# Kernel optimization log

Hardware: AMD Instinct MI355X
Metric: run time of the kernel (lower is better)

Reference implementation:

```python
import jax, jax.numpy as jnp
import numpy as np

B, V, N, S, F, H, K, STEPS = 8, 3, 400, 1200, 16, 32, 10, 12
ALPHA_FUSE = 0.8
NEG = -9e15


def setup_inputs() -> dict:
    key = jax.random.key(0)
    ks = jax.random.split(key, 16)
    g = lambda i, shape, s=0.1: jax.random.normal(ks[i], shape, jnp.float32) * s
    return {
        "feat": jax.random.normal(ks[0], (B, S, F), jnp.float32),
        "adj": jax.random.bernoulli(ks[1], 0.05, (B, V, S, S)).astype(jnp.float32),
        "dis_lab": jax.random.uniform(ks[2], (B, K), dtype=jnp.float32),
        "W_gat": g(3, (V, F, H), 0.3),
        "a_gat": g(4, (V, 2 * H, 1), 0.3),
        "qkv_W": g(5, (H, 3 * H)),
        "qkv_b": jnp.zeros((3 * H,), jnp.float32),
        "o_W": g(6, (H, H)),
        "o_b": jnp.zeros((H,), jnp.float32),
        "fus_W": g(7, (H, H)),
        "fus_b": jnp.zeros((H,), jnp.float32),
        "att1_W": g(8, (2 * H, H)),
        "att1_b": jnp.zeros((H,), jnp.float32),
        "att2_W": g(9, (H, 1)),
        "att2_b": jnp.zeros((1,), jnp.float32),
        "gru_Wih": g(10, (H, 3 * H)),
        "gru_Whh": g(11, (H, 3 * H)),
        "gru_bih": jnp.zeros((3 * H,), jnp.float32),
        "gru_bhh": jnp.zeros((3 * H,), jnp.float32),
        "out_W": g(12, (H, 1)),
        "out_b": jnp.zeros((1,), jnp.float32),
    }


def _forward(feat, adj, dis_lab, W_gat, a_gat, qkv_W, qkv_b, o_W, o_b,
             fus_W, fus_b, att1_W, att1_b, att2_W, att2_b,
             gru_Wih, gru_Whh, gru_bih, gru_bhh, out_W, out_b):
    # ---- per-view GAT (masked softmax over dense adjacency) ----
    Wh = jnp.einsum('bsf,vfh->bvsh', feat, W_gat)            # [B,V,S,H]
    a1, a2 = a_gat[:, :H, 0], a_gat[:, H:, 0]
    e = (jnp.einsum('bvsh,vh->bvs', Wh, a1)[..., :, None]
         + jnp.einsum('bvsh,vh->bvs', Wh, a2)[..., None, :])  # [B,V,S,S]
    e = jax.nn.leaky_relu(e, 0.2)
    e = jnp.where(adj > 0, e, NEG)
    att = jax.nn.softmax(e, axis=-1)
    hid = jax.nn.elu(jnp.einsum('bvst,bvth->bvsh', att, Wh))  # [B,V,S,H]
    # ---- cross-view self-attention fusion (single head) ----
    x = hid.reshape(B, V * S, H)
    q, k, v = jnp.split(x @ qkv_W + qkv_b, 3, axis=-1)
    logits = jnp.einsum('bld,bmd->blm', q, k) / jnp.sqrt(jnp.float32(H))
    sa = jnp.einsum('blm,bmd->bld', jax.nn.softmax(logits, axis=-1), v)
    sa = sa @ o_W + o_b
    hfuse = (ALPHA_FUSE * sa + (1.0 - ALPHA_FUSE) * x).reshape(B, V, S, H)
    gate = jax.nn.sigmoid(hfuse @ fus_W + fus_b)
    fusion = jnp.sum(gate * hfuse, axis=1)[:, 2 * N:, :]      # [B,N,H]
    # ---- attention over label stations ----
    label = fusion[:, :K, :]                                  # [B,K,H]
    unlabel = fusion[:, K, :]                                 # [B,H]
    cat = jnp.concatenate([label, jnp.broadcast_to(unlabel[:, None, :], label.shape)], axis=-1)
    s = jax.nn.relu(cat @ att1_W + att1_b) @ att2_W + att2_b  # [B,K,1]
    score = jax.nn.softmax(s[..., 0] * dis_lab, axis=1)
    ctx = jnp.einsum('bk,bkh->bh', score, label)
    # ---- GRU decoder (feed hidden state back as next input) ----
    def gru_cell(xt, h):
        gi = xt @ gru_Wih + gru_bih
        gh = h @ gru_Whh + gru_bhh
        ir, iz, inn = jnp.split(gi, 3, axis=-1)
        hr, hz, hn = jnp.split(gh, 3, axis=-1)
        r = jax.nn.sigmoid(ir + hr)
        z = jax.nn.sigmoid(iz + hz)
        n = jnp.tanh(inn + r * hn)
        return (1.0 - z) * n + z * h
    def step(carry, _):
        xt, h = carry
        h2 = gru_cell(xt, h)
        out = h2 @ out_W + out_b
        return (h2, h2), out[:, 0]
    _, outs = jax.lax.scan(step, (ctx, unlabel), None, length=STEPS)
    return outs.T  # [B, STEPS]


def reference(feat, adj, dis_lab, W_gat, a_gat, qkv_W, qkv_b, o_W, o_b,
              fus_W, fus_b, att1_W, att1_b, att2_W, att2_b,
              gru_Wih, gru_Whh, gru_bih, gru_bhh, out_W, out_b):
    return _forward(feat, adj, dis_lab, W_gat, a_gat, qkv_W, qkv_b, o_W, o_b,
                    fus_W, fus_b, att1_W, att1_b, att2_W, att2_b,
                    gru_Wih, gru_Whh, gru_bih, gru_bhh, out_W, out_b)
```

## Files before the change

### kernel.cpp

```cpp
#include <hip/hip_runtime.h>
#include <math.h>

#define Bb 8
#define Vv 3
#define Ss 1200
#define SgP 1280
#define Ff 16
#define Hh 32
#define Kk 10
#define STEPS 12
#define ROWS (Bb*Vv*Ss)
#define L (Vv*Ss)
#define KPAD 1280
#define NKB 160
#define MROW 40

typedef __attribute__((ext_vector_type(8))) short bf16x8;
typedef __attribute__((ext_vector_type(4))) float f32x4;
typedef __attribute__((ext_vector_type(4))) unsigned int u32x4;

__device__ __forceinline__ unsigned int pack_hi2(float x0, float x1) {
    return (__float_as_uint(x1) & 0xFFFF0000u) | (__float_as_uint(x0) >> 16);
}
__device__ __forceinline__ unsigned int pack_lo2(float x0, float x1) {
    float h0 = __uint_as_float(__float_as_uint(x0) & 0xFFFF0000u);
    float h1 = __uint_as_float(__float_as_uint(x1) & 0xFFFF0000u);
    return (__float_as_uint(x1 - h1) & 0xFFFF0000u) | (__float_as_uint(x0 - h0) >> 16);
}
__device__ __forceinline__ unsigned int spread4(unsigned int x) {
    x = (x | (x << 12)) & 0x000F000Fu;
    x = (x | (x << 6))  & 0x03030303u;
    x = (x | (x << 3))  & 0x11111111u;
    return x;
}

__global__ __launch_bounds__(256) void wh_wht_k(const float* __restrict__ feat,
                                                const float* __restrict__ W_gat,
                                                const float* __restrict__ a_gat,
                                                ushort* __restrict__ WhT,
                                                float* __restrict__ fvec,
                                                float* __restrict__ gvecP) {
    int bv = blockIdx.x / 20, t = blockIdx.x % 20;
    int b = bv / Vv, v = bv - b * Vv;
    int s0 = t * 64;
    int tid = threadIdx.x;

    __shared__ float T[64][33];
    __shared__ float Wg[16][32];
    for (int i = tid; i < 512; i += 256) Wg[i >> 5][i & 31] = W_gat[v * 512 + i];
    __syncthreads();

    int r8 = tid >> 5, h = tid & 31;
    float a1 = a_gat[v * 64 + h];
    float a2 = a_gat[v * 64 + 32 + h];
#pragma unroll
    for (int pass = 0; pass < 8; ++pass) {
        int s = s0 + pass * 8 + r8;
        float acc = 0.f;
        if (s < Ss) {
            const float4* fe = (const float4*)(feat + ((size_t)b * Ss + s) * Ff);
            float4 f0 = fe[0], f1 = fe[1], f2 = fe[2], f3 = fe[3];
            acc += f0.x * Wg[0][h]  + f0.y * Wg[1][h]  + f0.z * Wg[2][h]  + f0.w * Wg[3][h];
            acc += f1.x * Wg[4][h]  + f1.y * Wg[5][h]  + f1.z * Wg[6][h]  + f1.w * Wg[7][h];
            acc += f2.x * Wg[8][h]  + f2.y * Wg[9][h]  + f2.z * Wg[10][h] + f2.w * Wg[11][h];
            acc += f3.x * Wg[12][h] + f3.y * Wg[13][h] + f3.z * Wg[14][h] + f3.w * Wg[15][h];
        }
        T[pass * 8 + r8][h] = acc;
        float pf = acc * a1, pg = acc * a2;
#pragma unroll
        for (int m = 16; m >= 1; m >>= 1) {
            pf += __shfl_xor(pf, m);
            pg += __shfl_xor(pg, m);
        }
        if (h == 0 && s < Ss) {
            fvec[bv * Ss + s] = pf;
            gvecP[(size_t)bv * SgP + s] = pg;
        }
    }
    __syncthreads();

    int hh = tid >> 3, c = tid & 7;
    int kb = t * 8 + c;
    unsigned int hb[4], lb[4];
#pragma unroll
    for (int j = 0; j < 4; ++j) {
        float e0 = T[c * 8 + 2 * j][hh], e1 = T[c * 8 + 2 * j + 1][hh];
        hb[j] = pack_hi2(e0, e1);
        lb[j] = pack_lo2(e0, e1);
    }
    size_t base = (((size_t)bv * NKB + kb) * 2) * 256 + hh * 8;
    *(uint4*)(WhT + base)       = make_uint4(hb[0], hb[1], hb[2], hb[3]);
    *(uint4*)(WhT + base + 256) = make_uint4(lb[0], lb[1], lb[2], lb[3]);
}

__global__ __launch_bounds__(256) void gmax_k(float* __restrict__ gvecP,
                                              float* __restrict__ Gmax) {
    int bv = blockIdx.x;
    int tid = threadIdx.x;
    if (tid < SgP - Ss) gvecP[(size_t)bv * SgP + Ss + tid] = 0.f;
    float m = -3.0e38f;
    for (int t = tid; t < Ss; t += 256) m = fmaxf(m, gvecP[(size_t)bv * SgP + t]);
#pragma unroll
    for (int mm = 32; mm >= 1; mm >>= 1) m = fmaxf(m, __shfl_xor(m, mm));
    __shared__ float red[4];
    if ((tid & 63) == 0) red[tid >> 6] = m;
    __syncthreads();
    if (tid == 0) Gmax[bv] = fmaxf(fmaxf(red[0], red[1]), fmaxf(red[2], red[3]));
}

__global__ __launch_bounds__(256) void adj_pack_k(const float* __restrict__ adj,
                                                  unsigned int* __restrict__ maskb) {
    int gw = (blockIdx.x * 256 + threadIdx.x) >> 6;
    int lane = threadIdx.x & 63;
    for (int row = gw; row < ROWS; row += 5760) {
        const float* ar = adj + (size_t)row * Ss;
        unsigned int* mrow = maskb + (size_t)row * MROW;
        float4 a[5];
#pragma unroll
        for (int c = 0; c < 5; ++c) {
            int base = c * 256 + lane * 4;
            a[c] = (base + 3 < Ss) ? *(const float4*)(ar + base)
                                   : make_float4(0.f, 0.f, 0.f, 0.f);
        }
#pragma unroll
        for (int c = 0; c < 5; ++c) {
            unsigned long long b0 = __ballot(a[c].x > 0.f);
            unsigned long long b1 = __ballot(a[c].y > 0.f);
            unsigned long long b2 = __ballot(a[c].z > 0.f);
            unsigned long long b3 = __ballot(a[c].w > 0.f);
            int nw = (c == 4) ? 6 : 8;
            if (lane < nw) {
                int sh = 8 * lane;
                unsigned int B0 = (unsigned int)(b0 >> sh) & 0xFFu;
                unsigned int B1 = (unsigned int)(b1 >> sh) & 0xFFu;
                unsigned int B2 = (unsigned int)(b2 >> sh) & 0xFFu;
                unsigned int B3 = (unsigned int)(b3 >> sh) & 0xFFu;
                mrow[c * 8 + lane] = spread4(B0) | (spread4(B1) << 1)
                                   | (spread4(B2) << 2) | (spread4(B3) << 3);
            }
        }
        if (lane < 2) mrow[38 + lane] = 0u;
    }
}

__global__ __launch_bounds__(256, 4) void gat_mfma_k(const unsigned int* __restrict__ maskb,
                                                     const ushort* __restrict__ WhT,
                                                     const float* __restrict__ fvec,
                                                     const float* __restrict__ gvecP,
                                                     const float* __restrict__ Gmax,
                                                     float* __restrict__ hid,
                                                     float* __restrict__ hsel) {
    int blk = blockIdx.x;
    int bv = blk / 75, tb = blk % 75;
    int wk = threadIdx.x >> 6, lane = threadIdx.x & 63;
    int rowbase = tb * 16;
    int lr = lane & 15, kg = lane >> 4;
    int b = bv / Vv, v = bv - b * Vv;

    int ar = rowbase + lr;
    const float* g_b = gvecP + (size_t)bv * SgP;
    float fr = fvec[bv * Ss + ar];
    float M = fr + Gmax[bv];
    float Mr = fmaxf(M, 0.2f * M);

    const unsigned int* mrow = maskb + (size_t)(bv * Ss + ar) * MROW + wk * 10;
    unsigned int mw[10];
#pragma unroll
    for (int i = 0; i < 5; ++i) {
        uint2 t = *(const uint2*)(mrow + 2 * i);
        mw[2 * i] = t.x; mw[2 * i + 1] = t.y;
    }

    f32x4 acc0 = {0.f, 0.f, 0.f, 0.f}, acc1 = {0.f, 0.f, 0.f, 0.f};
    float psum = 0.f;
    const ushort* Wbv = WhT + ((size_t)bv * NKB) * 512;

    int kst = wk * 320;
#pragma unroll
    for (int s = 0; s < 10; ++s) {
        int t0 = kst + s * 32 + kg * 8;
        int kb = t0 >> 3;
        unsigned int mb = (mw[s] >> (kg * 8)) & 0xFFu;

        const ushort* Bp = Wbv + (size_t)kb * 512 + lr * 8;
        bf16x8 bh0 = *(const bf16x8*)(Bp);
        bf16x8 bh1 = *(const bf16x8*)(Bp + 128);
        bf16x8 bl0 = *(const bf16x8*)(Bp + 256);
        bf16x8 bl1 = *(const bf16x8*)(Bp + 384);

        float4 gA = *(const float4*)(g_b + t0);
        float4 gB = *(const float4*)(g_b + t0 + 4);
        float gv8[8] = {gA.x, gA.y, gA.z, gA.w, gB.x, gB.y, gB.z, gB.w};
        float p[8];
#pragma unroll
        for (int j = 0; j < 8; ++j) {
            float e = fr + gv8[j];
            e = fmaxf(e, 0.2f * e);
            float pe = __expf(e - Mr);
            p[j] = ((mb >> j) & 1u) ? pe : 0.f;
            psum += p[j];
        }
        unsigned int hbp[4], lbp[4];
#pragma unroll
        for (int j = 0; j < 4; ++j) {
            hbp[j] = pack_hi2(p[2 * j], p[2 * j + 1]);
            lbp[j] = pack_lo2(p[2 * j], p[2 * j + 1]);
        }
        bf16x8 ah = __builtin_bit_cast(bf16x8, (u32x4){hbp[0], hbp[1], hbp[2], hbp[3]});
        bf16x8 al = __builtin_bit_cast(bf16x8, (u32x4){lbp[0], lbp[1], lbp[2], lbp[3]});
        acc0 = __builtin_amdgcn_mfma_f32_16x16x32_bf16(ah, bh0, acc0, 0, 0, 0);
        acc0 = __builtin_amdgcn_mfma_f32_16x16x32_bf16(ah, bl0, acc0, 0, 0, 0);
        acc0 = __builtin_amdgcn_mfma_f32_16x16x32_bf16(al, bh0, acc0, 0, 0, 0);
        acc1 = __builtin_amdgcn_mfma_f32_16x16x32_bf16(ah, bh1, acc1, 0, 0, 0);
        acc1 = __builtin_amdgcn_mfma_f32_16x16x32_bf16(ah, bl1, acc1, 0, 0, 0);
        acc1 = __builtin_amdgcn_mfma_f32_16x16x32_bf16(al, bh1, acc1, 0, 0, 0);
    }

    psum += __shfl_xor(psum, 16);
    psum += __shfl_xor(psum, 32);

    __shared__ float accS[4][2][16][17];
    __shared__ float psS[4][16];
#pragma unroll
    for (int j = 0; j < 4; ++j) {
        accS[wk][0][kg * 4 + j][lr] = acc0[j];
        accS[wk][1][kg * 4 + j][lr] = acc1[j];
    }
    if (lane < 16) psS[wk][lr] = psum;
    __syncthreads();
    if (threadIdx.x < 16)
        psS[0][threadIdx.x] += psS[1][threadIdx.x] + psS[2][threadIdx.x] + psS[3][threadIdx.x];
    __syncthreads();

    bool qb = (tb == 50);
    for (int idx = threadIdx.x; idx < 512; idx += 256) {
        int r = idx >> 5, col = idx & 31, tt = col >> 4, c = col & 15;
        float a = accS[0][tt][r][c] + accS[1][tt][r][c] + accS[2][tt][r][c] + accS[3][tt][r][c];
        float rr = a / psS[0][r];
        float hv = (rr > 0.f) ? rr : expm1f(rr);
        hid[((size_t)bv * Ss + rowbase + r) * 32 + col] = hv;
        if (qb && r < 11) hsel[(((size_t)b * Vv + v) * 11 + r) * 32 + col] = hv;
    }
}

__global__ __launch_bounds__(256) void attn_q_k(const float* __restrict__ hsel,
                                                const float* __restrict__ qkv_W,
                                                const float* __restrict__ qkv_b,
                                                float* __restrict__ qt,
                                                float* __restrict__ qc) {
    int b = blockIdx.x;
    int tid = threadIdx.x;
    __shared__ float hq[33][33];
    __shared__ float W1[32][33];
    __shared__ float W2[32][33];
    __shared__ float qS[33][33];

    for (int idx = tid; idx < 33 * 32; idx += 256) {
        int q = idx >> 5, i = idx & 31;
        int si = q / 3, v = q - si * 3;
        hq[q][i] = hsel[(((size_t)b * Vv + v) * 11 + si) * 32 + i];
    }
    for (int idx = tid; idx < 1024; idx += 256) {
        int i = idx >> 5, j = idx & 31;
        W1[i][j] = qkv_W[i * 96 + j];
        W2[i][j] = qkv_W[i * 96 + 32 + j];
    }
    __syncthreads();
    for (int idx = tid; idx < 33 * 32; idx += 256) {
        int q = idx >> 5, j = idx & 31;
        float a = qkv_b[j];
#pragma unroll
        for (int i = 0; i < 32; ++i) a += hq[q][i] * W1[i][j];
        qS[q][j] = a;
    }
    __syncthreads();
    for (int idx = tid; idx < 33 * 32; idx += 256) {
        int q = idx >> 5, i = idx & 31;
        float a = 0.f;
#pragma unroll
        for (int j = 0; j < 32; ++j) a += qS[q][j] * W2[i][j];
        qt[(size_t)b * 33 * 32 + q * 32 + i] = a;
    }
    if (tid < 33) {
        float a = 0.f;
        for (int j = 0; j < 32; ++j) a += qS[tid][j] * qkv_b[32 + j];
        qc[b * 33 + tid] = a;
    }
}

#define CH 120
#define NCH 30
#define PREC 34
__global__ __launch_bounds__(256) void attn_part_k(const float* __restrict__ hid,
                                                   const float* __restrict__ qt,
                                                   const float* __restrict__ qc,
                                                   float* __restrict__ part) {
    int blk = blockIdx.x;
    int b = blk / NCH, ch = blk % NCH;
    int k0 = ch * CH;
    int tid = threadIdx.x;
    const float inv = 0.1767766952966369f;

    __shared__ float hC[CH][33];
    __shared__ float qtS[33][33];
    __shared__ float qcS[33];
    __shared__ float lS[33][124];
    __shared__ float mS[33], lsS[33];

    for (int idx = tid; idx < CH * 32; idx += 256) {
        int r = idx >> 5, i = idx & 31;
        hC[r][i] = hid[((size_t)b * L + k0 + r) * 32 + i];
    }
    for (int idx = tid; idx < 33 * 32; idx += 256) {
        int q = idx >> 5, i = idx & 31;
        qtS[q][i] = qt[(size_t)b * 33 * 32 + q * 32 + i];
    }
    if (tid < 33) qcS[tid] = qc[b * 33 + tid];
    __syncthreads();

    for (int idx = tid; idx < 33 * CH; idx += 256) {
        int q = idx / CH, m = idx - q * CH;
        float d = 0.f;
#pragma unroll
        for (int i = 0; i < 32; ++i) d += qtS[q][i] * hC[m][i];
        lS[q][m] = (d + qcS[q]) * inv;
    }
    __syncthreads();

    int q4 = tid >> 2, j4 = tid & 3;
    if (q4 < 33) {
        float m = -3.0e38f;
        for (int k = j4; k < CH; k += 4) m = fmaxf(m, lS[q4][k]);
        m = fmaxf(m, __shfl_xor(m, 1));
        m = fmaxf(m, __shfl_xor(m, 2));
        float ssum = 0.f;
        for (int k = j4; k < CH; k += 4) {
            float p = __expf(lS[q4][k] - m);
            lS[q4][k] = p;
            ssum += p;
        }
        ssum += __shfl_xor(ssum, 1);
        ssum += __shfl_xor(ssum, 2);
        if (j4 == 0) { mS[q4] = m; lsS[q4] = ssum; }
    }
    __syncthreads();

    float* po = part + ((size_t)b * NCH + ch) * (33 * PREC);
    for (int idx = tid; idx < 33 * 32; idx += 256) {
        int q = idx >> 5, hh = idx & 31;
        float a = 0.f;
        for (int k = 0; k < CH; k += 4) {
            float4 p4 = *(const float4*)&lS[q][k];
            a += p4.x * hC[k][hh] + p4.y * hC[k+1][hh] + p4.z * hC[k+2][hh] + p4.w * hC[k+3][hh];
        }
        po[q * PREC + hh] = a;
    }
    if (tid < 33) { po[tid * PREC + 32] = mS[tid]; po[tid * PREC + 33] = lsS[tid]; }
}

__global__ __launch_bounds__(256) void attn_comb_k(const float* __restrict__ part,
                                                   const float* __restrict__ hsel,
                                                   const float* __restrict__ qkv_W,
                                                   const float* __restrict__ qkv_b,
                                                   const float* __restrict__ o_W,
                                                   const float* __restrict__ o_b,
                                                   const float* __restrict__ fus_W,
                                                   const float* __restrict__ fus_b,
                                                   float* __restrict__ hfg) {
    int b = blockIdx.x;
    int tid = threadIdx.x;
    __shared__ float RS[33][NCH];
    __shared__ float LSs[33];
    __shared__ float oS[33][33];
    __shared__ float vS[33][33];
    __shared__ float hfS[33][33];
    const float* pb = part + (size_t)b * NCH * (33 * PREC);

    if (tid < 33) {
        float M = -3.0e38f;
        for (int c = 0; c < NCH; ++c) M = fmaxf(M, pb[c * 33 * PREC + tid * PREC + 32]);
        float Lt = 0.f;
        for (int c = 0; c < NCH; ++c) {
            float w = __expf(pb[c * 33 * PREC + tid * PREC + 32] - M);
            RS[tid][c] = w;
            Lt += w * pb[c * 33 * PREC + tid * PREC + 33];
        }
        LSs[tid] = Lt;
    }
    __syncthreads();

    for (int idx = tid; idx < 33 * 32; idx += 256) {
        int q = idx >> 5, hh = idx & 31;
        float a = 0.f;
        for (int c = 0; c < NCH; ++c) a += RS[q][c] * pb[c * 33 * PREC + q * PREC + hh];
        oS[q][hh] = a / LSs[q];
    }
    __syncthreads();
    for (int idx = tid; idx < 33 * 32; idx += 256) {
        int q = idx >> 5, j = idx & 31;
        float a = qkv_b[64 + j];
#pragma unroll
        for (int i = 0; i < 32; ++i) a += oS[q][i] * qkv_W[i * 96 + 64 + j];
        vS[q][j] = a;
    }
    __syncthreads();
    for (int idx = tid; idx < 33 * 32; idx += 256) {
        int q = idx >> 5, hh = idx & 31;
        int si = q / 3, v = q - si * 3;
        float o = o_b[hh];
#pragma unroll
        for (int i = 0; i < 32; ++i) o += vS[q][i] * o_W[i * 32 + hh];
        float x = hsel[(((size_t)b * Vv + v) * 11 + si) * Hh + hh];
        hfS[q][hh] = 0.8f * o + 0.2f * x;
    }
    __syncthreads();
    for (int idx = tid; idx < 33 * 32; idx += 256) {
        int q = idx >> 5, hh = idx & 31;
        float gacc = fus_b[hh];
#pragma unroll
        for (int i = 0; i < 32; ++i) gacc += hfS[q][i] * fus_W[i * 32 + hh];
        float gate = 1.f / (1.f + __expf(-gacc));
        hfg[(size_t)(b * 33 + q) * 32 + hh] = gate * hfS[q][hh];
    }
}

__global__ __launch_bounds__(64) void head_k(const float* __restrict__ hfg,
                                             const float* __restrict__ dis_lab,
                                             const float* __restrict__ att1_W,
                                             const float* __restrict__ att1_b,
                                             const float* __restrict__ att2_W,
                                             const float* __restrict__ att2_b,
                                             const float* __restrict__ Wih,
                                             const float* __restrict__ Whh,
                                             const float* __restrict__ bih,
                                             const float* __restrict__ bhh,
                                             const float* __restrict__ out_W,
                                             const float* __restrict__ out_b,
                                             float* __restrict__ out) {
    int b = blockIdx.x;
    int tid = threadIdx.x;
    int j = tid & 31, half = tid >> 5;

    __shared__ float lab[11][32];
    __shared__ float a1T[32][68];
    __shared__ float WihT[3][32][36];
    __shared__ float WhhT[3][32][36];
    __shared__ float sc[12];
    __shared__ float xS[32], hS[32];

    for (int i = tid; i < 352; i += 64) {
        int k = i >> 5, hh = i & 31;
        float val = 0.f;
#pragma unroll
        for (int v = 0; v < 3; ++v) val += hfg[(size_t)(b * 33 + k * 3 + v) * 32 + hh];
        lab[k][hh] = val;
    }
    for (int idx = tid; idx < 2048; idx += 64) {
        int i = idx >> 5, jj = idx & 31;
        a1T[jj][i] = att1_W[idx];
    }
    for (int idx = tid; idx < 3072; idx += 64) {
        int i = idx / 96, col = idx - i * 96;
        int g = col >> 5, jj = col & 31;
        WihT[g][jj][i] = Wih[idx];
        WhhT[g][jj][i] = Whh[idx];
    }
    __syncthreads();

    float a2w = att2_W[j];
    float a1b = att1_b[j];
    float a2b = att2_b[0];
#pragma unroll
    for (int kk = 0; kk < 5; ++kk) {
        int k = 2 * kk + half;
        float t1 = a1b;
#pragma unroll
        for (int c = 0; c < 8; ++c) {
            float4 lb4 = *(const float4*)&lab[k][c * 4];
            float4 w4  = *(const float4*)&a1T[j][c * 4];
            t1 += lb4.x * w4.x + lb4.y * w4.y + lb4.z * w4.z + lb4.w * w4.w;
        }
#pragma unroll
        for (int c = 0; c < 8; ++c) {
            float4 lb4 = *(const float4*)&lab[10][c * 4];
            float4 w4  = *(const float4*)&a1T[j][32 + c * 4];
            t1 += lb4.x * w4.x + lb4.y * w4.y + lb4.z * w4.z + lb4.w * w4.w;
        }
        float val = fmaxf(t1, 0.f) * a2w;
#pragma unroll
        for (int mm = 16; mm >= 1; mm >>= 1) val += __shfl_xor(val, mm);
        if (j == 0) sc[k] = (val + a2b) * dis_lab[b * Kk + k];
    }
    __syncthreads();
    if (tid == 0) {
        float mx = sc[0];
        for (int k = 1; k < 10; ++k) mx = fmaxf(mx, sc[k]);
        float sm = 0.f;
        for (int k = 0; k < 10; ++k) { sc[k] = __expf(sc[k] - mx); sm += sc[k]; }
        for (int k = 0; k < 10; ++k) sc[k] /= sm;
    }
    __syncthreads();
    if (tid < 32) {
        float c = 0.f;
        for (int k = 0; k < 10; ++k) c += sc[k] * lab[k][tid];
        xS[tid] = c;
        hS[tid] = lab[10][tid];
    }
    __syncthreads();

    float b_ir = bih[j], b_iz = bih[32 + j], b_in = bih[64 + j];
    float b_hr = bhh[j], b_hz = bhh[32 + j], b_hn = bhh[64 + j];
    float ow = out_W[j], ob = out_b[0];
    int i0 = half * 16;

    for (int t = 0; t < STEPS; ++t) {
        float gi_r = 0.f, gi_z = 0.f, gi_n = 0.f;
        float gh_r = 0.f, gh_z = 0.f, gh_n = 0.f;
#pragma unroll
        for (int c = 0; c < 4; ++c) {
            float4 x4 = *(const float4*)&xS[i0 + c * 4];
            float4 h4 = *(const float4*)&hS[i0 + c * 4];
            float4 wr = *(const float4*)&WihT[0][j][i0 + c * 4];
            float4 wz = *(const float4*)&WihT[1][j][i0 + c * 4];
            float4 wn = *(const float4*)&WihT[2][j][i0 + c * 4];
            float4 ur = *(const float4*)&WhhT[0][j][i0 + c * 4];
            float4 uz = *(const float4*)&WhhT[1][j][i0 + c * 4];
            float4 un = *(const float4*)&WhhT[2][j][i0 + c * 4];
            gi_r += x4.x * wr.x + x4.y * wr.y + x4.z * wr.z + x4.w * wr.w;
            gi_z += x4.x * wz.x + x4.y * wz.y + x4.z * wz.z + x4.w * wz.w;
            gi_n += x4.x * wn.x + x4.y * wn.y + x4.z * wn.z + x4.w * wn.w;
            gh_r += h4.x * ur.x + h4.y * ur.y + h4.z * ur.z + h4.w * ur.w;
            gh_z += h4.x * uz.x + h4.y * uz.y + h4.z * uz.z + h4.w * uz.w;
            gh_n += h4.x * un.x + h4.y * un.y + h4.z * un.z + h4.w * un.w;
        }
        gi_r += __shfl_xor(gi_r, 32); gi_z += __shfl_xor(gi_z, 32); gi_n += __shfl_xor(gi_n, 32);
        gh_r += __shfl_xor(gh_r, 32); gh_z += __shfl_xor(gh_z, 32); gh_n += __shfl_xor(gh_n, 32);

        float hprev = hS[j];
        float r = 1.f / (1.f + __expf(-(gi_r + b_ir + gh_r + b_hr)));
        float z = 1.f / (1.f + __expf(-(gi_z + b_iz + gh_z + b_hz)));
        float n = tanhf(gi_n + b_in + r * (gh_n + b_hn));
        float hnew = (1.f - z) * n + z * hprev;

        float outp = hnew * ow;
#pragma unroll
        for (int mm = 16; mm >= 1; mm >>= 1) outp += __shfl_xor(outp, mm);
        if (tid == 0) out[b * STEPS + t] = outp + ob;
        __syncthreads();
        if (tid < 32) { hS[tid] = hnew; xS[tid] = hnew; }
        __syncthreads();
    }
}

extern "C" void kernel_launch(void* const* d_in, const int* in_sizes, int n_in,
                              void* d_out, int out_size, void* d_ws, size_t ws_size,
                              hipStream_t stream) {
    const float* feat    = (const float*)d_in[0];
    const float* adj     = (const float*)d_in[1];
    const float* dis_lab = (const float*)d_in[2];
    const float* W_gat   = (const float*)d_in[3];
    const float* a_gat   = (const float*)d_in[4];
    const float* qkv_W   = (const float*)d_in[5];
    const float* qkv_b   = (const float*)d_in[6];
    const float* o_W     = (const float*)d_in[7];
    const float* o_b     = (const float*)d_in[8];
    const float* fus_W   = (const float*)d_in[9];
    const float* fus_b   = (const float*)d_in[10];
    const float* att1_W  = (const float*)d_in[11];
    const float* att1_b  = (const float*)d_in[12];
    const float* att2_W  = (const float*)d_in[13];
    const float* att2_b  = (const float*)d_in[14];
    const float* Wih     = (const float*)d_in[15];
    const float* Whh     = (const float*)d_in[16];
    const float* bih     = (const float*)d_in[17];
    const float* bhh     = (const float*)d_in[18];
    const float* out_W   = (const float*)d_in[19];
    const float* out_b   = (const float*)d_in[20];
    float* out = (float*)d_out;

    float* ws = (float*)d_ws;
    float*  hid    = ws;
    float*  fvec   = ws + 921600;
    float*  gvecP  = ws + 950400;
    float*  Gmax   = ws + 981120;
    ushort* WhT    = (ushort*)(ws + 981152);
    float*  part   = ws + 981152;
    float*  hsel   = ws + 1964192;
    float*  hfg    = ws + 1972640;
    float*  qt     = ws + 1981088;
    float*  qc     = ws + 1989536;
    unsigned int* maskb = (unsigned int*)(ws + 1989824);

    adj_pack_k<<<dim3(1440), dim3(256), 0, stream>>>(adj, maskb);
    wh_wht_k<<<dim3(Bb * Vv * 20), dim3(256), 0, stream>>>(feat, W_gat, a_gat,
                                                           WhT, fvec, gvecP);
    gmax_k<<<dim3(Bb * Vv), dim3(256), 0, stream>>>(gvecP, Gmax);
    gat_mfma_k<<<dim3(Bb * Vv * 75), dim3(256), 0, stream>>>(maskb, WhT,
                                                             fvec, gvecP, Gmax, hid, hsel);
    attn_q_k<<<dim3(Bb), dim3(256), 0, stream>>>(hsel, qkv_W, qkv_b, qt, qc);
    attn_part_k<<<dim3(Bb * NCH), dim3(256), 0, stream>>>(hid, qt, qc, part);
    attn_comb_k<<<dim3(Bb), dim3(256), 0, stream>>>(part, hsel, qkv_W, qkv_b,
                                                    o_W, o_b, fus_W, fus_b, hfg);
    head_k<<<dim3(Bb), dim3(64), 0, stream>>>(hfg, dis_lab, att1_W, att1_b, att2_W, att2_b,
                                              Wih, Whh, bih, bhh, out_W, out_b, out);
}
```

Baseline: 130.0 us.

## Fold gmax into wh kernel via atomicMax and fuse combine with head

```diff
diff --git a/kernel.cpp b/kernel.cpp
--- a/kernel.cpp
+++ b/kernel.cpp
@@ -33,83 +33,18 @@
     x = (x | (x << 3))  & 0x11111111u;
     return x;
 }
-
-__global__ __launch_bounds__(256) void wh_wht_k(const float* __restrict__ feat,
-                                                const float* __restrict__ W_gat,
-                                                const float* __restrict__ a_gat,
-                                                ushort* __restrict__ WhT,
-                                                float* __restrict__ fvec,
-                                                float* __restrict__ gvecP) {
-    int bv = blockIdx.x / 20, t = blockIdx.x % 20;
-    int b = bv / Vv, v = bv - b * Vv;
-    int s0 = t * 64;
-    int tid = threadIdx.x;
-
-    __shared__ float T[64][33];
-    __shared__ float Wg[16][32];
-    for (int i = tid; i < 512; i += 256) Wg[i >> 5][i & 31] = W_gat[v * 512 + i];
-    __syncthreads();
-
-    int r8 = tid >> 5, h = tid & 31;
-    float a1 = a_gat[v * 64 + h];
-    float a2 = a_gat[v * 64 + 32 + h];
-#pragma unroll
-    for (int pass = 0; pass < 8; ++pass) {
-        int s = s0 + pass * 8 + r8;
-        float acc = 0.f;
-        if (s < Ss) {
-            const float4* fe = (const float4*)(feat + ((size_t)b * Ss + s) * Ff);
-            float4 f0 = fe[0], f1 = fe[1], f2 = fe[2], f3 = fe[3];
-            acc += f0.x * Wg[0][h]  + f0.y * Wg[1][h]  + f0.z * Wg[2][h]  + f0.w * Wg[3][h];
-            acc += f1.x * Wg[4][h]  + f1.y * Wg[5][h]  + f1.z * Wg[6][h]  + f1.w * Wg[7][h];
-            acc += f2.x * Wg[8][h]  + f2.y * Wg[9][h]  + f2.z * Wg[10][h] + f2.w * Wg[11][h];
-            acc += f3.x * Wg[12][h] + f3.y * Wg[13][h] + f3.z * Wg[14][h] + f3.w * Wg[15][h];
-        }
-        T[pass * 8 + r8][h] = acc;
-        float pf = acc * a1, pg = acc * a2;
-#pragma unroll
-        for (int m = 16; m >= 1; m >>= 1) {
-            pf += __shfl_xor(pf, m);
-            pg += __shfl_xor(pg, m);
-        }
-        if (h == 0 && s < Ss) {
-            fvec[bv * Ss + s] = pf;
-            gvecP[(size_t)bv * SgP + s] = pg;
-        }
-    }
-    __syncthreads();
-
-    int hh = tid >> 3, c = tid & 7;
-    int kb = t * 8 + c;
-    unsigned int hb[4], lb[4];
-#pragma unroll
-    for (int j = 0; j < 4; ++j) {
-        float e0 = T[c * 8 + 2 * j][hh], e1 = T[c * 8 + 2 * j + 1][hh];
-        hb[j] = pack_hi2(e0, e1);
-        lb[j] = pack_lo2(e0, e1);
-    }
-    size_t base = (((size_t)bv * NKB + kb) * 2) * 256 + hh * 8;
-    *(uint4*)(WhT + base)       = make_uint4(hb[0], hb[1], hb[2], hb[3]);
-    *(uint4*)(WhT + base + 256) = make_uint4(lb[0], lb[1], lb[2], lb[3]);
-}
-
-__global__ __launch_bounds__(256) void gmax_k(float* __restrict__ gvecP,
-                                              float* __restrict__ Gmax) {
-    int bv = blockIdx.x;
-    int tid = threadIdx.x;
-    if (tid < SgP - Ss) gvecP[(size_t)bv * SgP + Ss + tid] = 0.f;
-    float m = -3.0e38f;
-    for (int t = tid; t < Ss; t += 256) m = fmaxf(m, gvecP[(size_t)bv * SgP + t]);
-#pragma unroll
-    for (int mm = 32; mm >= 1; mm >>= 1) m = fmaxf(m, __shfl_xor(m, mm));
-    __shared__ float red[4];
-    if ((tid & 63) == 0) red[tid >> 6] = m;
-    __syncthreads();
-    if (tid == 0) Gmax[bv] = fmaxf(fmaxf(red[0], red[1]), fmaxf(red[2], red[3]));
+__device__ __forceinline__ unsigned int enc_f(float f) {
+    unsigned int u = __float_as_uint(f);
+    return (u >> 31) ? ~u : (u | 0x80000000u);
+}
+__device__ __forceinline__ float dec_f(unsigned int e) {
+    return (e >> 31) ? __uint_as_float(e & 0x7FFFFFFFu) : __uint_as_float(~e);
 }
 
 __global__ __launch_bounds__(256) void adj_pack_k(const float* __restrict__ adj,
-                                                  unsigned int* __restrict__ maskb) {
+                                                  unsigned int* __restrict__ maskb,
+                                                  unsigned int* __restrict__ GmaxE) {
+    if (blockIdx.x == 0 && threadIdx.x < Bb * Vv) GmaxE[threadIdx.x] = 0u;
     int gw = (blockIdx.x * 256 + threadIdx.x) >> 6;
     int lane = threadIdx.x & 63;
     for (int row = gw; row < ROWS; row += 5760) {
@@ -143,11 +78,80 @@
     }
 }
 
+__global__ __launch_bounds__(256) void wh_wht_k(const float* __restrict__ feat,
+                                                const float* __restrict__ W_gat,
+                                                const float* __restrict__ a_gat,
+                                                ushort* __restrict__ WhT,
+                                                float* __restrict__ fvec,
+                                                float* __restrict__ gvecP,
+                                                unsigned int* __restrict__ GmaxE) {
+    int bv = blockIdx.x / 20, t = blockIdx.x % 20;
+    int b = bv / Vv, v = bv - b * Vv;
+    int s0 = t * 64;
+    int tid = threadIdx.x;
+
+    __shared__ float T[64][33];
+    __shared__ float Wg[16][32];
+    __shared__ float gred[8];
+    for (int i = tid; i < 512; i += 256) Wg[i >> 5][i & 31] = W_gat[v * 512 + i];
+    __syncthreads();
+
+    int r8 = tid >> 5, h = tid & 31;
+    float a1 = a_gat[v * 64 + h];
+    float a2 = a_gat[v * 64 + 32 + h];
+    float myg = -3.0e38f;
+#pragma unroll
+    for (int pass = 0; pass < 8; ++pass) {
+        int s = s0 + pass * 8 + r8;
+        float acc = 0.f;
+        if (s < Ss) {
+            const float4* fe = (const float4*)(feat + ((size_t)b * Ss + s) * Ff);
+            float4 f0 = fe[0], f1 = fe[1], f2 = fe[2], f3 = fe[3];
+            acc += f0.x * Wg[0][h]  + f0.y * Wg[1][h]  + f0.z * Wg[2][h]  + f0.w * Wg[3][h];
+            acc += f1.x * Wg[4][h]  + f1.y * Wg[5][h]  + f1.z * Wg[6][h]  + f1.w * Wg[7][h];
+            acc += f2.x * Wg[8][h]  + f2.y * Wg[9][h]  + f2.z * Wg[10][h] + f2.w * Wg[11][h];
+            acc += f3.x * Wg[12][h] + f3.y * Wg[13][h] + f3.z * Wg[14][h] + f3.w * Wg[15][h];
+        }
+        T[pass * 8 + r8][h] = acc;
+        float pf = acc * a1, pg = acc * a2;
+#pragma unroll
+        for (int m = 16; m >= 1; m >>= 1) {
+            pf += __shfl_xor(pf, m);
+            pg += __shfl_xor(pg, m);
+        }
+        if (h == 0) {
+            if (s < Ss) { fvec[bv * Ss + s] = pf; myg = fmaxf(myg, pg); }
+            gvecP[(size_t)bv * SgP + s] = (s < Ss) ? pg : 0.f;
+        }
+    }
+    if (h == 0) gred[r8] = myg;
+    __syncthreads();
+    if (tid == 0) {
+        float m = gred[0];
+#pragma unroll
+        for (int i = 1; i < 8; ++i) m = fmaxf(m, gred[i]);
+        atomicMax(&GmaxE[bv], enc_f(m));
+    }
+
+    int hh = tid >> 3, c = tid & 7;
+    int kb = t * 8 + c;
+    unsigned int hb[4], lb[4];
+#pragma unroll
+    for (int j = 0; j < 4; ++j) {
+        float e0 = T[c * 8 + 2 * j][hh], e1 = T[c * 8 + 2 * j + 1][hh];
+        hb[j] = pack_hi2(e0, e1);
+        lb[j] = pack_lo2(e0, e1);
+    }
+    size_t base = (((size_t)bv * NKB + kb) * 2) * 256 + hh * 8;
+    *(uint4*)(WhT + base)       = make_uint4(hb[0], hb[1], hb[2], hb[3]);
+    *(uint4*)(WhT + base + 256) = make_uint4(lb[0], lb[1], lb[2], lb[3]);
+}
+
 __global__ __launch_bounds__(256, 4) void gat_mfma_k(const unsigned int* __restrict__ maskb,
                                                      const ushort* __restrict__ WhT,
                                                      const float* __restrict__ fvec,
                                                      const float* __restrict__ gvecP,
-                                                     const float* __restrict__ Gmax,
+                                                     const unsigned int* __restrict__ GmaxE,
                                                      float* __restrict__ hid,
                                                      float* __restrict__ hsel) {
     int blk = blockIdx.x;
@@ -160,7 +164,7 @@
     int ar = rowbase + lr;
     const float* g_b = gvecP + (size_t)bv * SgP;
     float fr = fvec[bv * Ss + ar];
-    float M = fr + Gmax[bv];
+    float M = fr + dec_f(GmaxE[bv]);
     float Mr = fmaxf(M, 0.2f * M);
 
     const unsigned int* mrow = maskb + (size_t)(bv * Ss + ar) * MROW + wk * 10;
@@ -358,7 +362,7 @@
     if (tid < 33) { po[tid * PREC + 32] = mS[tid]; po[tid * PREC + 33] = lsS[tid]; }
 }
 
-__global__ __launch_bounds__(256) void attn_comb_k(const float* __restrict__ part,
+__global__ __launch_bounds__(256) void comb_head_k(const float* __restrict__ part,
                                                    const float* __restrict__ hsel,
                                                    const float* __restrict__ qkv_W,
                                                    const float* __restrict__ qkv_b,
@@ -366,7 +370,18 @@
                                                    const float* __restrict__ o_b,
                                                    const float* __restrict__ fus_W,
                                                    const float* __restrict__ fus_b,
-                                                   float* __restrict__ hfg) {
+                                                   const float* __restrict__ dis_lab,
+                                                   const float* __restrict__ att1_W,
+                                                   const float* __restrict__ att1_b,
+                                                   const float* __restrict__ att2_W,
+                                                   const float* __restrict__ att2_b,
+                                                   const float* __restrict__ Wih,
+                                                   const float* __restrict__ Whh,
+                                                   const float* __restrict__ bih,
+                                                   const float* __restrict__ bhh,
+                                                   const float* __restrict__ out_W,
+                                                   const float* __restrict__ out_b,
+                                                   float* __restrict__ out) {
     int b = blockIdx.x;
     int tid = threadIdx.x;
     __shared__ float RS[33][NCH];
@@ -374,6 +389,14 @@
     __shared__ float oS[33][33];
     __shared__ float vS[33][33];
     __shared__ float hfS[33][33];
+    __shared__ float hfgS[33][32];
+    __shared__ float lab[11][32];
+    __shared__ float a1T[32][68];
+    __shared__ float WihT[3][32][36];
+    __shared__ float WhhT[3][32][36];
+    __shared__ float sc[12];
+    __shared__ float xS[32], hS[32];
+
     const float* pb = part + (size_t)b * NCH * (33 * PREC);
 
     if (tid < 33) {
@@ -420,46 +443,19 @@
 #pragma unroll
         for (int i = 0; i < 32; ++i) gacc += hfS[q][i] * fus_W[i * 32 + hh];
         float gate = 1.f / (1.f + __expf(-gacc));
-        hfg[(size_t)(b * 33 + q) * 32 + hh] = gate * hfS[q][hh];
-    }
-}
-
-__global__ __launch_bounds__(64) void head_k(const float* __restrict__ hfg,
-                                             const float* __restrict__ dis_lab,
-                                             const float* __restrict__ att1_W,
-                                             const float* __restrict__ att1_b,
-                                             const float* __restrict__ att2_W,
-                                             const float* __restrict__ att2_b,
-                                             const float* __restrict__ Wih,
-                                             const float* __restrict__ Whh,
-                                             const float* __restrict__ bih,
-                                             const float* __restrict__ bhh,
-                                             const float* __restrict__ out_W,
-                                             const float* __restrict__ out_b,
-                                             float* __restrict__ out) {
-    int b = blockIdx.x;
-    int tid = threadIdx.x;
-    int j = tid & 31, half = tid >> 5;
-
-    __shared__ float lab[11][32];
-    __shared__ float a1T[32][68];
-    __shared__ float WihT[3][32][36];
-    __shared__ float WhhT[3][32][36];
-    __shared__ float sc[12];
-    __shared__ float xS[32], hS[32];
-
-    for (int i = tid; i < 352; i += 64) {
+        hfgS[q][hh] = gate * hfS[q][hh];
+    }
+    __syncthreads();
+
+    for (int i = tid; i < 352; i += 256) {
         int k = i >> 5, hh = i & 31;
-        float val = 0.f;
-#pragma unroll
-        for (int v = 0; v < 3; ++v) val += hfg[(size_t)(b * 33 + k * 3 + v) * 32 + hh];
-        lab[k][hh] = val;
-    }
-    for (int idx = tid; idx < 2048; idx += 64) {
+        lab[k][hh] = hfgS[k * 3 + 0][hh] + hfgS[k * 3 + 1][hh] + hfgS[k * 3 + 2][hh];
+    }
+    for (int idx = tid; idx < 2048; idx += 256) {
         int i = idx >> 5, jj = idx & 31;
         a1T[jj][i] = att1_W[idx];
     }
-    for (int idx = tid; idx < 3072; idx += 64) {
+    for (int idx = tid; idx < 3072; idx += 256) {
         int i = idx / 96, col = idx - i * 96;
         int g = col >> 5, jj = col & 31;
         WihT[g][jj][i] = Wih[idx];
@@ -467,29 +463,32 @@
     }
     __syncthreads();
 
-    float a2w = att2_W[j];
-    float a1b = att1_b[j];
-    float a2b = att2_b[0];
-#pragma unroll
-    for (int kk = 0; kk < 5; ++kk) {
-        int k = 2 * kk + half;
-        float t1 = a1b;
-#pragma unroll
-        for (int c = 0; c < 8; ++c) {
-            float4 lb4 = *(const float4*)&lab[k][c * 4];
-            float4 w4  = *(const float4*)&a1T[j][c * 4];
-            t1 += lb4.x * w4.x + lb4.y * w4.y + lb4.z * w4.z + lb4.w * w4.w;
-        }
-#pragma unroll
-        for (int c = 0; c < 8; ++c) {
-            float4 lb4 = *(const float4*)&lab[10][c * 4];
-            float4 w4  = *(const float4*)&a1T[j][32 + c * 4];
-            t1 += lb4.x * w4.x + lb4.y * w4.y + lb4.z * w4.z + lb4.w * w4.w;
-        }
-        float val = fmaxf(t1, 0.f) * a2w;
-#pragma unroll
-        for (int mm = 16; mm >= 1; mm >>= 1) val += __shfl_xor(val, mm);
-        if (j == 0) sc[k] = (val + a2b) * dis_lab[b * Kk + k];
+    int j = tid & 31, half = (tid >> 5) & 1;
+    if (tid < 64) {
+        float a2w = att2_W[j];
+        float a1b = att1_b[j];
+        float a2b = att2_b[0];
+#pragma unroll
+        for (int kk = 0; kk < 5; ++kk) {
+            int k = 2 * kk + half;
+            float t1 = a1b;
+#pragma unroll
+            for (int c = 0; c < 8; ++c) {
+                float4 lb4 = *(const float4*)&lab[k][c * 4];
+                float4 w4  = *(const float4*)&a1T[j][c * 4];
+                t1 += lb4.x * w4.x + lb4.y * w4.y + lb4.z * w4.z + lb4.w * w4.w;
+            }
+#pragma unroll
+            for (int c = 0; c < 8; ++c) {
+                float4 lb4 = *(const float4*)&lab[10][c * 4];
+                float4 w4  = *(const float4*)&a1T[j][32 + c * 4];
+                t1 += lb4.x * w4.x + lb4.y * w4.y + lb4.z * w4.z + lb4.w * w4.w;
+            }
+            float val = fmaxf(t1, 0.f) * a2w;
+#pragma unroll
+            for (int mm = 16; mm >= 1; mm >>= 1) val += __shfl_xor(val, mm);
+            if (j == 0) sc[k] = (val + a2b) * dis_lab[b * Kk + k];
+        }
     }
     __syncthreads();
     if (tid == 0) {
@@ -514,40 +513,48 @@
     int i0 = half * 16;
 
     for (int t = 0; t < STEPS; ++t) {
-        float gi_r = 0.f, gi_z = 0.f, gi_n = 0.f;
-        float gh_r = 0.f, gh_z = 0.f, gh_n = 0.f;
-#pragma unroll
-        for (int c = 0; c < 4; ++c) {
-            float4 x4 = *(const float4*)&xS[i0 + c * 4];
-            float4 h4 = *(const float4*)&hS[i0 + c * 4];
-            float4 wr = *(const float4*)&WihT[0][j][i0 + c * 4];
-            float4 wz = *(const float4*)&WihT[1][j][i0 + c * 4];
-            float4 wn = *(const float4*)&WihT[2][j][i0 + c * 4];
-            float4 ur = *(const float4*)&WhhT[0][j][i0 + c * 4];
-            float4 uz = *(const float4*)&WhhT[1][j][i0 + c * 4];
-            float4 un = *(const float4*)&WhhT[2][j][i0 + c * 4];
-            gi_r += x4.x * wr.x + x4.y * wr.y + x4.z * wr.z + x4.w * wr.w;
-            gi_z += x4.x * wz.x + x4.y * wz.y + x4.z * wz.z + x4.w * wz.w;
-            gi_n += x4.x * wn.x + x4.y * wn.y + x4.z * wn.z + x4.w * wn.w;
-            gh_r += h4.x * ur.x + h4.y * ur.y + h4.z * ur.z + h4.w * ur.w;
-            gh_z += h4.x * uz.x + h4.y * uz.y + h4.z * uz.z + h4.w * uz.w;
-            gh_n += h4.x * un.x + h4.y * un.y + h4.z * un.z + h4.w * un.w;
-        }
-        gi_r += __shfl_xor(gi_r, 32); gi_z += __shfl_xor(gi_z, 32); gi_n += __shfl_xor(gi_n, 32);
-        gh_r += __shfl_xor(gh_r, 32); gh_z += __shfl_xor(gh_z, 32); gh_n += __shfl_xor(gh_n, 32);
-
-        float hprev = hS[j];
-        float r = 1.f / (1.f + __expf(-(gi_r + b_ir + gh_r + b_hr)));
-        float z = 1.f / (1.f + __expf(-(gi_z + b_iz + gh_z + b_hz)));
-        float n = tanhf(gi_n + b_in + r * (gh_n + b_hn));
-        float hnew = (1.f - z) * n + z * hprev;
-
-        float outp = hnew * ow;
-#pragma unroll
-        for (int mm = 16; mm >= 1; mm >>= 1) outp += __shfl_xor(outp, mm);
-        if (tid == 0) out[b * STEPS + t] = outp + ob;
+        if (tid < 64) {
+            float gi_r = 0.f, gi_z = 0.f, gi_n = 0.f;
+            float gh_r = 0.f, gh_z = 0.f, gh_n = 0.f;
+#pragma unroll
+            for (int c = 0; c < 4; ++c) {
+                float4 x4 = *(const float4*)&xS[i0 + c * 4];
+                float4 h4 = *(const float4*)&hS[i0 + c * 4];
+                float4 wr = *(const float4*)&WihT[0][j][i0 + c * 4];
+                float4 wz = *(const float4*)&WihT[1][j][i0 + c * 4];
+                float4 wn = *(const float4*)&WihT[2][j][i0 + c * 4];
+                float4 ur = *(const float4*)&WhhT[0][j][i0 + c * 4];
+                float4 uz = *(const float4*)&WhhT[1][j][i0 + c * 4];
+                float4 un = *(const float4*)&WhhT[2][j][i0 + c * 4];
+                gi_r += x4.x * wr.x + x4.y * wr.y + x4.z * wr.z + x4.w * wr.w;
+                gi_z += x4.x * wz.x + x4.y * wz.y + x4.z * wz.z + x4.w * wz.w;
+                gi_n += x4.x * wn.x + x4.y * wn.y + x4.z * wn.z + x4.w * wn.w;
+                gh_r += h4.x * ur.x + h4.y * ur.y + h4.z * ur.z + h4.w * ur.w;
+                gh_z += h4.x * uz.x + h4.y * uz.y + h4.z * uz.z + h4.w * uz.w;
+                gh_n += h4.x * un.x + h4.y * un.y + h4.z * un.z + h4.w * un.w;
+            }
+            gi_r += __shfl_xor(gi_r, 32); gi_z += __shfl_xor(gi_z, 32); gi_n += __shfl_xor(gi_n, 32);
+            gh_r += __shfl_xor(gh_r, 32); gh_z += __shfl_xor(gh_z, 32); gh_n += __shfl_xor(gh_n, 32);
+
+            float hprev = hS[j];
+            float r = 1.f / (1.f + __expf(-(gi_r + b_ir + gh_r + b_hr)));
+            float z = 1.f / (1.f + __expf(-(gi_z + b_iz + gh_z + b_hz)));
+            float n = tanhf(gi_n + b_in + r * (gh_n + b_hn));
+            float hnew = (1.f - z) * n + z * hprev;
+
+            float outp = hnew * ow;
+#pragma unroll
+            for (int mm = 16; mm >= 1; mm >>= 1) outp += __shfl_xor(outp, mm);
+            if (tid == 0) out[b * STEPS + t] = outp + ob;
+            if (tid < 32) { xS[32 + 0] = 0.f; }
+            if (tid < 32) {  }
+            if (tid < 32) { sc[11] = hnew; }
+            if (tid < 32) { hS[j] = hS[j]; }
+            if (tid < 32) { xS[j] = xS[j]; }
+            if (tid < 32) { oS[0][j] = hnew; }
+        }
         __syncthreads();
-        if (tid < 32) { hS[tid] = hnew; xS[tid] = hnew; }
+        if (tid < 32) { hS[tid] = oS[0][tid]; xS[tid] = oS[0][tid]; }
         __syncthreads();
     }
 }
@@ -582,25 +589,23 @@
     float*  hid    = ws;
     float*  fvec   = ws + 921600;
     float*  gvecP  = ws + 950400;
-    float*  Gmax   = ws + 981120;
+    unsigned int* GmaxE = (unsigned int*)(ws + 981120);
     ushort* WhT    = (ushort*)(ws + 981152);
     float*  part   = ws + 981152;
     float*  hsel   = ws + 1964192;
-    float*  hfg    = ws + 1972640;
-    float*  qt     = ws + 1981088;
-    float*  qc     = ws + 1989536;
-    unsigned int* maskb = (unsigned int*)(ws + 1989824);
-
-    adj_pack_k<<<dim3(1440), dim3(256), 0, stream>>>(adj, maskb);
+    float*  qt     = ws + 1972640;
+    float*  qc     = ws + 1981088;
+    unsigned int* maskb = (unsigned int*)(ws + 1981376);
+
+    adj_pack_k<<<dim3(1440), dim3(256), 0, stream>>>(adj, maskb, GmaxE);
     wh_wht_k<<<dim3(Bb * Vv * 20), dim3(256), 0, stream>>>(feat, W_gat, a_gat,
-                                                           WhT, fvec, gvecP);
-    gmax_k<<<dim3(Bb * Vv), dim3(256), 0, stream>>>(gvecP, Gmax);
+                                                           WhT, fvec, gvecP, GmaxE);
     gat_mfma_k<<<dim3(Bb * Vv * 75), dim3(256), 0, stream>>>(maskb, WhT,
-                                                             fvec, gvecP, Gmax, hid, hsel);
+                                                             fvec, gvecP, GmaxE, hid, hsel);
     attn_q_k<<<dim3(Bb), dim3(256), 0, stream>>>(hsel, qkv_W, qkv_b, qt, qc);
     attn_part_k<<<dim3(Bb * NCH), dim3(256), 0, stream>>>(hid, qt, qc, part);
-    attn_comb_k<<<dim3(Bb), dim3(256), 0, stream>>>(part, hsel, qkv_W, qkv_b,
-                                                    o_W, o_b, fus_W, fus_b, hfg);
-    head_k<<<dim3(Bb), dim3(64), 0, stream>>>(hfg, dis_lab, att1_W, att1_b, att2_W, att2_b,
-                                              Wih, Whh, bih, bhh, out_W, out_b, out);
-}
+    comb_head_k<<<dim3(Bb), dim3(256), 0, stream>>>(part, hsel, qkv_W, qkv_b,
+                                                    o_W, o_b, fus_W, fus_b,
+                                                    dis_lab, att1_W, att1_b, att2_W, att2_b,
+                                                    Wih, Whh, bih, bhh, out_W, out_b, out);
+}
```

Result: faster. 124.8 us (-4.0%).
